# Kernel optimization log

Hardware: AMD Instinct MI355X
Metric: run time of the kernel (lower is better)

Reference implementation:

```python
import jax, jax.numpy as jnp
import numpy as np

S, B, C = 7, 2, 20
LAMBDA_COORD = 5.0
LAMBDA_NOOBJ = 0.5
WH_EPS = 1e-6
IOU_EPS = 1e-6
BATCH = 16384


def _iou_yolo(a, b):
    # a, b: [..., 4] in (cx, cy, w, h) 'yolo' center format
    ax1, ay1 = a[..., 0] - a[..., 2] / 2, a[..., 1] - a[..., 3] / 2
    ax2, ay2 = a[..., 0] + a[..., 2] / 2, a[..., 1] + a[..., 3] / 2
    bx1, by1 = b[..., 0] - b[..., 2] / 2, b[..., 1] - b[..., 3] / 2
    bx2, by2 = b[..., 0] + b[..., 2] / 2, b[..., 1] + b[..., 3] / 2
    iw = jnp.clip(jnp.minimum(ax2, bx2) - jnp.maximum(ax1, bx1), 0.0)
    ih = jnp.clip(jnp.minimum(ay2, by2) - jnp.maximum(ay1, by1), 0.0)
    inter = iw * ih
    area_a = jnp.abs((ax2 - ax1) * (ay2 - ay1))
    area_b = jnp.abs((bx2 - bx1) * (by2 - by1))
    return inter / (area_a + area_b - inter + IOU_EPS)


def setup_inputs() -> dict:
    key = jax.random.key(0)
    k1, k2, k3 = jax.random.split(key, 3)
    D = C + 5 * B  # 30
    y_trues = jax.random.uniform(k1, (BATCH, S, S, D), dtype=jnp.float32)
    # conf channel must be exactly 0.0 or 1.0 (loss branches on == 1)
    conf = (jax.random.uniform(k2, (BATCH, S, S)) < 0.3).astype(jnp.float32)
    y_trues = y_trues.at[..., 4].set(conf)
    y_preds = jax.random.normal(k3, (BATCH, S, S, D), dtype=jnp.float32)
    return {"y_trues": y_trues, "y_preds": y_preds}


def reference(y_trues, y_preds):
    D = C + 5 * B
    t = y_trues.reshape(-1, S * S, D)   # [N, 49, 30]
    p = y_preds.reshape(-1, S * S, D)
    batch_size = p.shape[0]

    b = t[..., 0:4]
    bhat1 = p[..., 0:4]
    bhat2 = p[..., 5:9]

    iou1 = _iou_yolo(b, bhat1)          # [N, 49]
    iou2 = _iou_yolo(b, bhat2)
    use1 = iou1 > iou2

    bhat = jnp.where(use1[..., None], bhat1, bhat2)            # responsible box
    confhat_chosen = jnp.where(use1, p[..., 4], p[..., 9])
    confhat_other = jnp.where(use1, p[..., 9], p[..., 4])

    # coord losses (object cells)
    xy = LAMBDA_COORD * ((b[..., 0] - bhat[..., 0]) ** 2 + (b[..., 1] - bhat[..., 1]) ** 2)
    wh = LAMBDA_COORD * (
        (jnp.sqrt(b[..., 2]) - jnp.sqrt(jnp.abs(bhat[..., 2] + WH_EPS))) ** 2
        + (jnp.sqrt(b[..., 3]) - jnp.sqrt(jnp.abs(bhat[..., 3] + WH_EPS))) ** 2
    )
    obj_conf = (t[..., 4] - confhat_chosen) ** 2
    noobj_in_obj = LAMBDA_NOOBJ * (0.0 - confhat_other) ** 2
    cls = jnp.sum((t[..., 10:] - p[..., 10:]) ** 2, axis=-1)

    obj_terms = xy + wh + obj_conf + noobj_in_obj + cls

    # no-object cells: penalize both predicted confs toward y_true conf (== target conf channel)
    noobj_terms = LAMBDA_NOOBJ * (
        (t[..., 4] - p[..., 4]) ** 2 + (t[..., 4] - p[..., 9]) ** 2
    )

    obj_mask = t[..., 4] == 1.0
    total = jnp.sum(jnp.where(obj_mask, obj_terms, noobj_terms))
    return total / batch_size
```

## Files before the change

### kernel.cpp

```cpp
#include <hip/hip_runtime.h>

#define LAMBDA_COORD 5.0f
#define LAMBDA_NOOBJ 0.5f
#define WH_EPS 1e-6f
#define IOU_EPS 1e-6f


constexpr int THREADS = 256;
constexpr int TILE_VEC4 = 1920;

__device__ __forceinline__ float iou_yolo(float a0, float a1, float a2, float a3,
                                          float b0, float b1, float b2, float b3) {
    float ax1 = a0 - a2 * 0.5f, ay1 = a1 - a3 * 0.5f;
    float ax2 = a0 + a2 * 0.5f, ay2 = a1 + a3 * 0.5f;
    float bx1 = b0 - b2 * 0.5f, by1 = b1 - b3 * 0.5f;
    float bx2 = b0 + b2 * 0.5f, by2 = b1 + b3 * 0.5f;
    float iw = fmaxf(fminf(ax2, bx2) - fmaxf(ax1, bx1), 0.0f);
    float ih = fmaxf(fminf(ay2, by2) - fmaxf(ay1, by1), 0.0f);
    float inter = iw * ih;
    float area_a = fabsf((ax2 - ax1) * (ay2 - ay1));
    float area_b = fabsf((bx2 - bx1) * (by2 - by1));
    return inter / (area_a + area_b - inter + IOU_EPS);
}

__device__ __forceinline__ float cell_loss(const float* t, const float* p) {
    const float b0 = t[0], b1 = t[1], b2 = t[2], b3 = t[3], t4 = t[4];

    float iou1 = iou_yolo(b0, b1, b2, b3, p[0], p[1], p[2], p[3]);
    float iou2 = iou_yolo(b0, b1, b2, b3, p[5], p[6], p[7], p[8]);
    bool use1 = iou1 > iou2;

    float bh0 = use1 ? p[0] : p[5];
    float bh1 = use1 ? p[1] : p[6];
    float bh2 = use1 ? p[2] : p[7];
    float bh3 = use1 ? p[3] : p[8];
    float conf_c = use1 ? p[4] : p[9];
    float conf_o = use1 ? p[9] : p[4];

    float dx = b0 - bh0, dy = b1 - bh1;
    float xy = LAMBDA_COORD * (dx * dx + dy * dy);

    float sw = sqrtf(b2) - sqrtf(fabsf(bh2 + WH_EPS));
    float sh = sqrtf(b3) - sqrtf(fabsf(bh3 + WH_EPS));
    float wh = LAMBDA_COORD * (sw * sw + sh * sh);

    float dc = t4 - conf_c;
    float obj_conf = dc * dc;
    float noobj_in_obj = LAMBDA_NOOBJ * conf_o * conf_o;

    float cls = 0.0f;
#pragma unroll
    for (int k = 10; k < 30; ++k) {
        float d = t[k] - p[k];
        cls += d * d;
    }

    float obj_terms = xy + wh + obj_conf + noobj_in_obj + cls;

    float d4 = t4 - p[4], d9 = t4 - p[9];
    float noobj_terms = LAMBDA_NOOBJ * (d4 * d4 + d9 * d9);

    return (t4 == 1.0f) ? obj_terms : noobj_terms;
}

__device__ __forceinline__ void stage16(const float4* g_lane, float4* l_wave) {
    __builtin_amdgcn_global_load_lds(
        (const __attribute__((address_space(1))) void*)g_lane,
        (__attribute__((address_space(3))) void*)l_wave,
        16, 0, 0);
}

__global__ __launch_bounds__(THREADS, 2) void yolo_loss_main(
    const float4* __restrict__ tv, const float4* __restrict__ pv,
    float* __restrict__ ws) {
    __shared__ float4 sbuf[2 * TILE_VEC4];
    __shared__ float part[THREADS / 64];

    const int lane = threadIdx.x & 63;
    const int wid  = threadIdx.x >> 6;
    const size_t base = (size_t)blockIdx.x * TILE_VEC4;

#pragma unroll
    for (int j = 0; j < 15; ++j) {
        const int idx = j * THREADS + wid * 64;
        const int myidx = idx + lane;
        const float4* src = (myidx < TILE_VEC4)
                          ? (tv + base + myidx)
                          : (pv + base + (myidx - TILE_VEC4));
        stage16(src, sbuf + idx);
    }

    __syncthreads();

    const float* st = (const float*)sbuf;
    const float* sp = (const float*)(sbuf + TILE_VEC4);
    float v = cell_loss(st + threadIdx.x * 30, sp + threadIdx.x * 30);

#pragma unroll
    for (int off = 32; off > 0; off >>= 1)
        v += __shfl_down(v, off, 64);

    if (lane == 0) part[wid] = v;
    __syncthreads();
    if (threadIdx.x == 0) {
        float s = 0.0f;
#pragma unroll
        for (int w = 0; w < THREADS / 64; ++w) s += part[w];
        ws[blockIdx.x] = s;
    }
}

__global__ __launch_bounds__(256) void yolo_loss_finish(
    const float* __restrict__ ws, float* __restrict__ out,
    int nblocks, float inv_batch) {
    float v = 0.0f;
    for (int i = threadIdx.x; i < nblocks; i += 256) v += ws[i];
#pragma unroll
    for (int off = 32; off > 0; off >>= 1)
        v += __shfl_down(v, off, 64);
    __shared__ float part[4];
    if ((threadIdx.x & 63) == 0) part[threadIdx.x >> 6] = v;
    __syncthreads();
    if (threadIdx.x == 0)
        out[0] = (part[0] + part[1] + part[2] + part[3]) * inv_batch;
}

extern "C" void kernel_launch(void* const* d_in, const int* in_sizes, int n_in,
                              void* d_out, int out_size, void* d_ws, size_t ws_size,
                              hipStream_t stream) {
    const float* t = (const float*)d_in[0];
    const float* p = (const float*)d_in[1];
    float* out = (float*)d_out;
    float* ws = (float*)d_ws;

    const int total = in_sizes[0];
    const int cells = total / 30;
    const int batch = cells / 49;
    const float inv_batch = 1.0f / (float)batch;

    const int blocks = cells / THREADS;

    yolo_loss_main<<<blocks, THREADS, 0, stream>>>(
        (const float4*)t, (const float4*)p, ws);
    yolo_loss_finish<<<1, 256, 0, stream>>>(ws, out, blocks, inv_batch);
}
```

Measured before the change: 205.8 us.

## Load predictions directly into registers, stage only targets through LDS

Predictions are now read per thread as fifteen float2 loads straight into registers, and only the target tile is staged into shared memory with global_load_lds. This halves LDS usage per block and raises the launch-bounds occupancy hint from 2 to 5 blocks, aiming for more waves in flight to hide memory latency. The cost is strided, non-coalesced per-thread float2 loads from global memory (120-byte stride) and higher register pressure.

Result: no change. 206.1 us (+0.1%).

```diff
diff --git a/kernel.cpp b/kernel.cpp
--- a/kernel.cpp
+++ b/kernel.cpp
@@ -7,7 +7,7 @@
 
 
 constexpr int THREADS = 256;
-constexpr int TILE_VEC4 = 1920;
+constexpr int TILE_VEC4_T = 1920;
 
 __device__ __forceinline__ float iou_yolo(float a0, float a1, float a2, float a3,
                                           float b0, float b1, float b2, float b3) {
@@ -23,19 +23,21 @@
     return inter / (area_a + area_b - inter + IOU_EPS);
 }
 
-__device__ __forceinline__ float cell_loss(const float* t, const float* p) {
-    const float b0 = t[0], b1 = t[1], b2 = t[2], b3 = t[3], t4 = t[4];
-
-    float iou1 = iou_yolo(b0, b1, b2, b3, p[0], p[1], p[2], p[3]);
-    float iou2 = iou_yolo(b0, b1, b2, b3, p[5], p[6], p[7], p[8]);
+__device__ __forceinline__ float yolo_cell(
+    float b0, float b1, float b2, float b3, float t4,
+    float q0, float q1, float q2, float q3, float qc,
+    float r0, float r1, float r2, float r3, float rc,
+    float cls) {
+    float iou1 = iou_yolo(b0, b1, b2, b3, q0, q1, q2, q3);
+    float iou2 = iou_yolo(b0, b1, b2, b3, r0, r1, r2, r3);
     bool use1 = iou1 > iou2;
 
-    float bh0 = use1 ? p[0] : p[5];
-    float bh1 = use1 ? p[1] : p[6];
-    float bh2 = use1 ? p[2] : p[7];
-    float bh3 = use1 ? p[3] : p[8];
-    float conf_c = use1 ? p[4] : p[9];
-    float conf_o = use1 ? p[9] : p[4];
+    float bh0 = use1 ? q0 : r0;
+    float bh1 = use1 ? q1 : r1;
+    float bh2 = use1 ? q2 : r2;
+    float bh3 = use1 ? q3 : r3;
+    float conf_c = use1 ? qc : rc;
+    float conf_o = use1 ? rc : qc;
 
     float dx = b0 - bh0, dy = b1 - bh1;
     float xy = LAMBDA_COORD * (dx * dx + dy * dy);
@@ -48,16 +50,9 @@
     float obj_conf = dc * dc;
     float noobj_in_obj = LAMBDA_NOOBJ * conf_o * conf_o;
 
-    float cls = 0.0f;
-#pragma unroll
-    for (int k = 10; k < 30; ++k) {
-        float d = t[k] - p[k];
-        cls += d * d;
-    }
-
     float obj_terms = xy + wh + obj_conf + noobj_in_obj + cls;
 
-    float d4 = t4 - p[4], d9 = t4 - p[9];
+    float d4 = t4 - qc, d9 = t4 - rc;
     float noobj_terms = LAMBDA_NOOBJ * (d4 * d4 + d9 * d9);
 
     return (t4 == 1.0f) ? obj_terms : noobj_terms;
@@ -70,31 +65,55 @@
         16, 0, 0);
 }
 
-__global__ __launch_bounds__(THREADS, 2) void yolo_loss_main(
-    const float4* __restrict__ tv, const float4* __restrict__ pv,
+__global__ __launch_bounds__(THREADS, 5) void yolo_loss_main(
+    const float4* __restrict__ tv, const float2* __restrict__ pv,
     float* __restrict__ ws) {
-    __shared__ float4 sbuf[2 * TILE_VEC4];
+    __shared__ float4 sbuf[TILE_VEC4_T];
     __shared__ float part[THREADS / 64];
 
     const int lane = threadIdx.x & 63;
     const int wid  = threadIdx.x >> 6;
-    const size_t base = (size_t)blockIdx.x * TILE_VEC4;
+    const int cell = blockIdx.x * THREADS + threadIdx.x;
 
+    const float2* pg = pv + (size_t)cell * 15;
+    float2 q0 = pg[0],  q1 = pg[1],  q2 = pg[2],  q3 = pg[3],  q4 = pg[4];
+    float2 q5 = pg[5],  q6 = pg[6],  q7 = pg[7],  q8 = pg[8],  q9 = pg[9];
+    float2 q10 = pg[10], q11 = pg[11], q12 = pg[12], q13 = pg[13], q14 = pg[14];
+
+    const size_t tbase = (size_t)blockIdx.x * TILE_VEC4_T;
 #pragma unroll
-    for (int j = 0; j < 15; ++j) {
+    for (int j = 0; j < 7; ++j) {
         const int idx = j * THREADS + wid * 64;
-        const int myidx = idx + lane;
-        const float4* src = (myidx < TILE_VEC4)
-                          ? (tv + base + myidx)
-                          : (pv + base + (myidx - TILE_VEC4));
-        stage16(src, sbuf + idx);
+        stage16(tv + tbase + idx + lane, sbuf + idx);
+    }
+    if (wid < 2) {
+        const int idx = 7 * THREADS + wid * 64;
+        stage16(tv + tbase + idx + lane, sbuf + idx);
     }
 
     __syncthreads();
 
-    const float* st = (const float*)sbuf;
-    const float* sp = (const float*)(sbuf + TILE_VEC4);
-    float v = cell_loss(st + threadIdx.x * 30, sp + threadIdx.x * 30);
+    const float* t = (const float*)sbuf + threadIdx.x * 30;
+
+    float cls = 0.0f;
+    {
+        float d;
+        d = t[10] - q5.x;  cls += d * d;  d = t[11] - q5.y;  cls += d * d;
+        d = t[12] - q6.x;  cls += d * d;  d = t[13] - q6.y;  cls += d * d;
+        d = t[14] - q7.x;  cls += d * d;  d = t[15] - q7.y;  cls += d * d;
+        d = t[16] - q8.x;  cls += d * d;  d = t[17] - q8.y;  cls += d * d;
+        d = t[18] - q9.x;  cls += d * d;  d = t[19] - q9.y;  cls += d * d;
+        d = t[20] - q10.x; cls += d * d;  d = t[21] - q10.y; cls += d * d;
+        d = t[22] - q11.x; cls += d * d;  d = t[23] - q11.y; cls += d * d;
+        d = t[24] - q12.x; cls += d * d;  d = t[25] - q12.y; cls += d * d;
+        d = t[26] - q13.x; cls += d * d;  d = t[27] - q13.y; cls += d * d;
+        d = t[28] - q14.x; cls += d * d;  d = t[29] - q14.y; cls += d * d;
+    }
+
+    float v = yolo_cell(t[0], t[1], t[2], t[3], t[4],
+                        q0.x, q0.y, q1.x, q1.y, q2.x,
+                        q2.y, q3.x, q3.y, q4.x, q4.y,
+                        cls);
 
 #pragma unroll
     for (int off = 32; off > 0; off >>= 1)
@@ -141,6 +160,6 @@
     const int blocks = cells / THREADS;
 
     yolo_loss_main<<<blocks, THREADS, 0, stream>>>(
-        (const float4*)t, (const float4*)p, ws);
+        (const float4*)t, (const float2*)p, ws);
     yolo_loss_finish<<<1, 256, 0, stream>>>(ws, out, blocks, inv_batch);
 }
```
